# Performance work log

Measured on AMD Instinct MI355X. Metric: run time of the kernel, lower is better.

The kernel has to match this reference:

```python
import jax, jax.numpy as jnp
import numpy as np

N, T, NS, NO, HID, DENSE = 128, 1000, 10, 10, 64, 32


def setup_inputs() -> dict:
    key = jax.random.key(0)
    ks = jax.random.split(key, 16)
    s = 0.1  # init scale for RNN/dense weights
    inp = {
        "Yi_batch": jax.random.normal(ks[0], (N, T, NO), jnp.float32),
        "Xi_batch": jax.random.normal(ks[1], (N, T, NS), jnp.float32),
        # Kalman model parameters
        "H": 0.3 * jax.random.normal(ks[2], (NO, NS), jnp.float32),
        "mu_w": jnp.zeros((NO,), jnp.float32),
        "C_w": 0.1 * jnp.eye(NO, dtype=jnp.float32),
        # GRU parameters (torch layout: [3H, in])
        "W_ih": s * jax.random.normal(ks[3], (3 * HID, NO), jnp.float32),
        "W_hh": s * jax.random.normal(ks[4], (3 * HID, HID), jnp.float32),
        "b_ih": jnp.zeros((3 * HID,), jnp.float32),
        "b_hh": jnp.zeros((3 * HID,), jnp.float32),
        # dense head: fc -> relu -> {fc_mean, softplus(fc_vars)}
        "W_fc": s * jax.random.normal(ks[5], (DENSE, HID), jnp.float32),
        "b_fc": jnp.zeros((DENSE,), jnp.float32),
        "W_mean": s * jax.random.normal(ks[6], (NS, DENSE), jnp.float32),
        "b_mean": jnp.zeros((NS,), jnp.float32),
        "W_vars": s * jax.random.normal(ks[7], (NS, DENSE), jnp.float32),
        "b_vars": jnp.zeros((NS,), jnp.float32),
    }
    return inp


def _gru(x, W_ih, W_hh, b_ih, b_hh):
    # x: (N, T, in) -> (N, T, HID); torch GRU gate order: r, z, n
    xp = jnp.einsum('nti,gi->ntg', x, W_ih) + b_ih  # (N,T,3H)
    Hd = W_hh.shape[1]

    def step(h, xpt):
        gh = h @ W_hh.T + b_hh
        xr, xz, xn = jnp.split(xpt, 3, axis=-1)
        hr, hz, hn = jnp.split(gh, 3, axis=-1)
        r = jax.nn.sigmoid(xr + hr)
        z = jax.nn.sigmoid(xz + hz)
        n = jnp.tanh(xn + r * hn)
        h_new = (1.0 - z) * n + z * h
        return h_new, h_new

    h0 = jnp.zeros((x.shape[0], Hd), x.dtype)
    _, outs = jax.lax.scan(step, h0, jnp.swapaxes(xp, 0, 1))
    return jnp.swapaxes(outs, 0, 1)


def reference(Yi_batch, Xi_batch, H, mu_w, C_w,
              W_ih, W_hh, b_ih, b_hh,
              W_fc, b_fc, W_mean, b_mean, W_vars, b_vars):
    # --- RNN prior: mu_xt_yt_prev (N,T,NS), diagonal vars (N,T,NS) ---
    r_out = _gru(Yi_batch, W_ih, W_hh, b_ih, b_hh)
    y = jax.nn.relu(jnp.einsum('nth,dh->ntd', r_out, W_fc) + b_fc)
    mu_prev = jnp.einsum('ntd,sd->nts', y, W_mean) + b_mean          # (N,T,NS)
    vars_prev = jax.nn.softplus(jnp.einsum('ntd,sd->nts', y, W_vars) + b_vars)

    # --- posterior (Kalman update, L_prev diagonal) ---
    # S = H diag(v) H^T + C_w, per (n,t): (N,T,NO,NO)
    S = jnp.einsum('os,nts,ps->ntop', H, vars_prev, H) + C_w
    S_inv = jnp.linalg.inv(S)
    # K = diag(v) H^T S^{-1}: (N,T,NS,NO)
    K = jnp.einsum('nts,os,ntop->ntsp', vars_prev, H, S_inv)
    innov = Yi_batch - jnp.einsum('os,nts->nto', H, mu_prev)          # (N,T,NO)
    mu_post = mu_prev + jnp.einsum('ntso,nto->nts', K, innov)
    eye_s = jnp.eye(NS, dtype=vars_prev.dtype)
    L_post = vars_prev[..., :, None] * eye_s \
        - jnp.einsum('ntso,ntop,ntqp->ntsq', K, S, K)                 # (N,T,NS,NS)

    # --- Gaussian log-pdf of Xi_batch under N(mu_post, L_post) ---
    diff = Xi_batch - mu_post
    L_inv = jnp.linalg.inv(L_post)
    quad = jnp.einsum('nts,ntsq,ntq->nt', diff, L_inv, diff).sum(axis=1)
    logdet = jnp.linalg.slogdet(L_post)[1].sum(axis=1)
    # NOTE: faithful to source, including the + sign on the 2*pi term
    logprob = 0.5 * NS * T * jnp.log(jnp.asarray(2.0 * np.pi, diff.dtype)) \
        - 0.5 * logdet - 0.5 * quad                                   # (N,)
    return logprob.mean()
```

## Files before the change

kernel.cpp:

```cpp
#include <hip/hip_runtime.h>
#include <math.h>

#define N_    128
#define T_    1000
#define NS_   10
#define NO_   10
#define HID_  64
#define DENSE_ 32

typedef float v2f __attribute__((ext_vector_type(2)));
typedef float v4f __attribute__((ext_vector_type(4)));
typedef _Float16 h2v __attribute__((ext_vector_type(2)));

#define LDS_BARRIER() asm volatile("s_waitcnt lgkmcnt(0)\n\ts_barrier" ::: "memory")

#if __has_builtin(__builtin_amdgcn_fdot2)
#define FDOT2(acc, a, b) (acc) = __builtin_amdgcn_fdot2((a), (b), (acc), false)
#else
#define FDOT2(acc, a, b) asm("v_dot2_f32_f16 %0, %1, %2, %0" : "+v"(acc) : "v"(a), "v"(b))
#endif

__device__ __forceinline__ h2v pk_f16(float a, float b) {
    return __builtin_bit_cast(h2v, __builtin_amdgcn_cvt_pkrtz(a, b));
}

template <int CTRL>
__device__ __forceinline__ float dpp_mov(float x) {
    int r = __builtin_amdgcn_update_dpp(0, __builtin_bit_cast(int, x),
                                        CTRL, 0xF, 0xF, true);
    return __builtin_bit_cast(float, r);
}
__device__ __forceinline__ float quad_sum(float x) {
    x += dpp_mov<0xB1>(x);
    x += dpp_mov<0x4E>(x);
    return x;
}

__device__ __forceinline__ float fast_sigmoid(float x) {
    return __builtin_amdgcn_rcpf(1.f + __expf(-x));
}
__device__ __forceinline__ float fast_tanh(float x) {
    float e = __expf(2.f * x);
    return 1.f - 2.f * __builtin_amdgcn_rcpf(e + 1.f);
}

__global__ __launch_bounds__(256, 1) void gru_kernel(
    const float* __restrict__ Y,
    const float* __restrict__ W_ih,
    const float* __restrict__ W_hh,
    const float* __restrict__ b_ih,
    const float* __restrict__ b_hh,
    float* __restrict__ h_out,
    float* __restrict__ out)
{
    const int n    = blockIdx.x;
    const int tid  = threadIdx.x;
    const int w    = tid >> 6;
    const int l    = tid & 63;
    const int unit = w * 16 + (l >> 2);
    const int kh   = l & 3;

    if (n == 0 && tid == 0)
        out[0] = 0.5f * (float)NS_ * (float)T_ * logf(2.f * 3.14159265358979323846f);

    __shared__ __align__(16) h2v ylds[T_ * NO_ / 2];
    __shared__ __align__(16) _Float16 hbuf[HID_];

    const float* Yn = Y + (size_t)n * T_ * NO_;
    {
        const v2f* src = (const v2f*)Yn;
#pragma unroll 4
        for (int i = tid; i < T_ * NO_ / 2; i += 256) {
            v2f v = src[i];
            ylds[i] = pk_f16(v[0], v[1]);
        }
    }

    h2v whh[3][8];
#pragma unroll
    for (int g = 0; g < 3; ++g) {
        const v4f* wp = (const v4f*)(W_hh + (size_t)(g * HID_ + unit) * HID_ + kh * 16);
#pragma unroll
        for (int q = 0; q < 4; ++q) {
            v4f t = wp[q];
            whh[g][2 * q]     = pk_f16(t.x, t.y);
            whh[g][2 * q + 1] = pk_f16(t.z, t.w);
        }
    }
    h2v wihx[5];
    {
        const float s = (kh == 3) ? 0.f : 1.f;
        const int gx = (kh < 3) ? kh : 2;
        const v2f* ip = (const v2f*)(W_ih + (size_t)(gx * HID_ + unit) * NO_);
#pragma unroll
        for (int i = 0; i < 5; ++i) { v2f t = ip[i]; wihx[i] = pk_f16(t[0] * s, t[1] * s); }
    }
#pragma unroll
    for (int g = 0; g < 3; ++g)
#pragma unroll
        for (int k = 0; k < 8; ++k) asm volatile("" : "+v"(whh[g][k]));
#pragma unroll
    for (int i = 0; i < 5; ++i) asm volatile("" : "+v"(wihx[i]));

    const float mR = (kh == 0) ? 1.f : 0.f;
    const float mZ = (kh == 1) ? 1.f : 0.f;
    const float mN = (kh >= 2) ? 1.f : 0.f;
    const float cR = (kh == 0) ? (b_ih[unit] + b_hh[unit]) : 0.f;
    const float cZ = (kh == 0) ? (b_ih[HID_ + unit] + b_hh[HID_ + unit]) : 0.f;
    const float cN = (kh == 0) ? b_hh[2 * HID_ + unit] : 0.f;
    const float cX = (kh == 0) ? b_ih[2 * HID_ + unit] : 0.f;

    if (tid < HID_) hbuf[tid] = (_Float16)0.f;
    float h_own = 0.f;
    __syncthreads();

    float* hout = h_out + (size_t)n * T_ * HID_ + unit;

    h2v y0 = ylds[0], y1 = ylds[1], y2 = ylds[2], y3 = ylds[3], y4 = ylds[4];

    for (int t = 0; t < T_; ++t) {
        float xs = 0.f;
        FDOT2(xs, wihx[0], y0); FDOT2(xs, wihx[1], y1); FDOT2(xs, wihx[2], y2);
        FDOT2(xs, wihx[3], y3); FDOT2(xs, wihx[4], y4);

        float ar = cR, az = cZ, an = cN, xn = cX;
        const uint4* hp = (const uint4*)(hbuf + kh * 16);
        uint4 hq0 = hp[0], hq1 = hp[1];
        {
            h2v h0 = __builtin_bit_cast(h2v, hq0.x);
            h2v h1 = __builtin_bit_cast(h2v, hq0.y);
            h2v h2 = __builtin_bit_cast(h2v, hq0.z);
            h2v h3 = __builtin_bit_cast(h2v, hq0.w);
            FDOT2(ar, whh[0][0], h0); FDOT2(az, whh[1][0], h0); FDOT2(an, whh[2][0], h0);
            FDOT2(ar, whh[0][1], h1); FDOT2(az, whh[1][1], h1); FDOT2(an, whh[2][1], h1);
            FDOT2(ar, whh[0][2], h2); FDOT2(az, whh[1][2], h2); FDOT2(an, whh[2][2], h2);
            FDOT2(ar, whh[0][3], h3); FDOT2(az, whh[1][3], h3); FDOT2(an, whh[2][3], h3);
        }
        {
            h2v h0 = __builtin_bit_cast(h2v, hq1.x);
            h2v h1 = __builtin_bit_cast(h2v, hq1.y);
            h2v h2 = __builtin_bit_cast(h2v, hq1.z);
            h2v h3 = __builtin_bit_cast(h2v, hq1.w);
            FDOT2(ar, whh[0][4], h0); FDOT2(az, whh[1][4], h0); FDOT2(an, whh[2][4], h0);
            FDOT2(ar, whh[0][5], h1); FDOT2(az, whh[1][5], h1); FDOT2(an, whh[2][5], h1);
            FDOT2(ar, whh[0][6], h2); FDOT2(az, whh[1][6], h2); FDOT2(an, whh[2][6], h2);
            FDOT2(ar, whh[0][7], h3); FDOT2(az, whh[1][7], h3); FDOT2(an, whh[2][7], h3);
        }
        ar = fmaf(xs, mR, ar);
        az = fmaf(xs, mZ, az);
        xn = fmaf(xs, mN, xn);
        ar = quad_sum(ar);
        az = quad_sum(az);
        an = quad_sum(an);
        xn = quad_sum(xn);
        const float r  = fast_sigmoid(ar);
        const float z  = fast_sigmoid(az);
        const float nn = fast_tanh(xn + r * an);
        const float h_new = nn + z * (h_own - nn);
        h_own = h_new;
        if (kh == 0) {
            hbuf[unit] = (_Float16)h_new;
            hout[t * HID_] = h_new;
        }
        {
            const h2v* yrow = ylds + 5 * ((t + 1 < T_) ? t + 1 : t);
            y0 = yrow[0]; y1 = yrow[1]; y2 = yrow[2]; y3 = yrow[3]; y4 = yrow[4];
        }
        LDS_BARRIER();
    }
}

__global__ __launch_bounds__(256) void post_kernel(
    const float* __restrict__ h_out,
    const float* __restrict__ Y,
    const float* __restrict__ X,
    const float* __restrict__ Hm, const float* __restrict__ C_w,
    const float* __restrict__ W_fc, const float* __restrict__ b_fc,
    const float* __restrict__ W_mean, const float* __restrict__ b_mean,
    const float* __restrict__ W_vars, const float* __restrict__ b_vars,
    float* __restrict__ out)
{
    __shared__ float sWfc[DENSE_][HID_];
    __shared__ float sWm[NS_][DENSE_];
    __shared__ float sWv[NS_][DENSE_];
    __shared__ float sA[NS_][NO_];
    __shared__ float sM[NS_][NS_];
    __shared__ float sbfc[DENSE_], sbm[NS_], sbv[NS_];
    __shared__ float wsum[4];
    __shared__ float W[NO_][2 * NO_];
    __shared__ float fcol[NO_];

    const int tid = threadIdx.x;

    if (tid < NO_ * NO_) {
        const int i = tid / NO_, jj = tid % NO_;
        W[i][jj] = C_w[tid];
        W[i][NO_ + jj] = (i == jj) ? 1.f : 0.f;
    }
    __syncthreads();
    for (int p = 0; p < NO_; ++p) {
        const float ip = 1.f / W[p][p];
        __syncthreads();
        if (tid < 2 * NO_) W[p][tid] *= ip;
        __syncthreads();
        if (tid < NO_) fcol[tid] = (tid == p) ? 0.f : W[tid][p];
        __syncthreads();
        if (tid < NO_ * 2 * NO_) {
            const int i = tid / (2 * NO_), jj = tid % (2 * NO_);
            W[i][jj] -= fcol[i] * W[p][jj];
        }
        __syncthreads();
    }
    if (tid < NS_ * NO_) {
        const int s = tid / NO_, o = tid % NO_;
        float acc = 0.f;
        for (int p = 0; p < NO_; ++p) acc += Hm[p * NS_ + s] * W[p][NO_ + o];
        sA[s][o] = acc;
    }
    __syncthreads();
    if (tid < NS_ * NS_) {
        const int s = tid / NS_, q = tid % NS_;
        float acc = 0.f;
        for (int o = 0; o < NO_; ++o) acc += sA[s][o] * Hm[o * NS_ + q];
        sM[s][q] = acc;
    }

    for (int i = tid; i < DENSE_ * HID_; i += blockDim.x)
        sWfc[i / HID_][i % HID_] = W_fc[i];
    for (int i = tid; i < NS_ * DENSE_; i += blockDim.x) {
        sWm[i / DENSE_][i % DENSE_] = W_mean[i];
        sWv[i / DENSE_][i % DENSE_] = W_vars[i];
    }
    if (tid < DENSE_) sbfc[tid] = b_fc[tid];
    if (tid < NS_) { sbm[tid] = b_mean[tid]; sbv[tid] = b_vars[tid]; }
    __syncthreads();

    const int task = blockIdx.x * blockDim.x + tid;
    float contrib = 0.f;
    if (task < N_ * T_) {
        float y[DENSE_];
#pragma unroll
        for (int d = 0; d < DENSE_; ++d) y[d] = sbfc[d];
        const float* hp = h_out + (size_t)task * HID_;
#pragma unroll
        for (int k = 0; k < HID_; k += 4) {
            float4 h4 = *(const float4*)(hp + k);
#pragma unroll
            for (int d = 0; d < DENSE_; ++d) {
                y[d] += sWfc[d][k + 0] * h4.x + sWfc[d][k + 1] * h4.y +
                        sWfc[d][k + 2] * h4.z + sWfc[d][k + 3] * h4.w;
            }
        }
#pragma unroll
        for (int d = 0; d < DENSE_; ++d) y[d] = fmaxf(y[d], 0.f);

        float mu[NS_], vinv[NS_];
#pragma unroll
        for (int s = 0; s < NS_; ++s) {
            float am = sbm[s], av = sbv[s];
#pragma unroll
            for (int d = 0; d < DENSE_; ++d) { am += sWm[s][d] * y[d]; av += sWv[s][d] * y[d]; }
            mu[s] = am;
            float sp = (av > 20.f) ? av : log1pf(__expf(av));
            vinv[s] = 1.f / sp;
        }

        const float* yo = Y + (size_t)task * NO_;
        const float* xo = X + (size_t)task * NS_;
        float b[NS_];
#pragma unroll
        for (int s = 0; s < NS_; ++s) {
            float acc = vinv[s] * mu[s];
#pragma unroll
            for (int o = 0; o < NO_; ++o) acc += sA[s][o] * yo[o];
            b[s] = acc;
        }

        float L[NS_][NS_];
#pragma unroll
        for (int i = 0; i < NS_; ++i)
#pragma unroll
            for (int jj = 0; jj <= i; ++jj)
                L[i][jj] = sM[i][jj] + ((i == jj) ? vinv[i] : 0.f);
        float ld = 0.f;
        float dinv[NS_];
#pragma unroll
        for (int jj = 0; jj < NS_; ++jj) {
            float s = L[jj][jj];
#pragma unroll
            for (int k = 0; k < jj; ++k) s -= L[jj][k] * L[jj][k];
            float d = sqrtf(s);
            ld += __logf(d);
            float di = 1.f / d;
            dinv[jj] = di;
            L[jj][jj] = d;
#pragma unroll
            for (int i = jj + 1; i < NS_; ++i) {
                float t2 = L[i][jj];
#pragma unroll
                for (int k = 0; k < jj; ++k) t2 -= L[i][k] * L[jj][k];
                L[i][jj] = t2 * di;
            }
        }
        ld *= 2.f;

        float w[NS_];
#pragma unroll
        for (int i = 0; i < NS_; ++i) {
            float s = b[i];
#pragma unroll
            for (int k = 0; k < i; ++k) s -= L[i][k] * w[k];
            w[i] = s * dinv[i];
        }
        float mpost[NS_];
#pragma unroll
        for (int ii = NS_ - 1; ii >= 0; --ii) {
            float s = w[ii];
#pragma unroll
            for (int k = ii + 1; k < NS_; ++k) s -= L[k][ii] * mpost[k];
            mpost[ii] = s * dinv[ii];
        }

        float diff[NS_];
#pragma unroll
        for (int s = 0; s < NS_; ++s) diff[s] = xo[s] - mpost[s];
        float quad = 0.f;
#pragma unroll
        for (int jj = 0; jj < NS_; ++jj) {
            float u = 0.f;
#pragma unroll
            for (int i = jj; i < NS_; ++i) u += L[i][jj] * diff[i];
            quad += u * u;
        }

        contrib = 0.5f * (ld - quad) * (1.0f / (float)N_);
    }

#pragma unroll
    for (int off = 32; off; off >>= 1) contrib += __shfl_down(contrib, off);
    const int wid = tid >> 6;
    if ((tid & 63) == 0) wsum[wid] = contrib;
    __syncthreads();
    if (tid == 0) {
        float s = 0.f;
#pragma unroll
        for (int i = 0; i < 4; ++i) s += wsum[i];
        atomicAdd(out, s);
    }
}

extern "C" void kernel_launch(void* const* d_in, const int* in_sizes, int n_in,
                              void* d_out, int out_size, void* d_ws, size_t ws_size,
                              hipStream_t stream)
{
    const float* Y      = (const float*)d_in[0];
    const float* X      = (const float*)d_in[1];
    const float* H      = (const float*)d_in[2];
    const float* C_w    = (const float*)d_in[4];
    const float* W_ih   = (const float*)d_in[5];
    const float* W_hh   = (const float*)d_in[6];
    const float* b_ih   = (const float*)d_in[7];
    const float* b_hh   = (const float*)d_in[8];
    const float* W_fc   = (const float*)d_in[9];
    const float* b_fc   = (const float*)d_in[10];
    const float* W_mean = (const float*)d_in[11];
    const float* b_mean = (const float*)d_in[12];
    const float* W_vars = (const float*)d_in[13];
    const float* b_vars = (const float*)d_in[14];
    float* out = (float*)d_out;

    float* h_out = (float*)d_ws;

    hipLaunchKernelGGL(gru_kernel, dim3(N_), dim3(256), 0, stream,
                       Y, W_ih, W_hh, b_ih, b_hh, h_out, out);
    hipLaunchKernelGGL(post_kernel, dim3((N_ * T_ + 255) / 256), dim3(256), 0, stream,
                       h_out, Y, X, H, C_w, W_fc, b_fc, W_mean, b_mean,
                       W_vars, b_vars, out);
}
```

Measured before the change: 313.4 us.

## Pack two GRU sequences per 512-thread block sharing one barrier

Each GRU block now runs two batch sequences, one per 256-thread half, with separate LDS slices for Y and the hidden state. The grid drops from 128 to 64 blocks. The per-step workgroup barrier is now shared by 8 waves instead of 4, so each sequence can stall on the slower half. The intent is to put more waves per CU to hide the serial recurrence latency, or to pack sequences onto fewer CUs. On MI355X, which has more CUs than 128, this halves the number of active CUs and couples the two sequences through the barrier.

```diff
diff --git a/kernel.cpp b/kernel.cpp
--- a/kernel.cpp
+++ b/kernel.cpp
@@ -44,7 +44,7 @@
     return 1.f - 2.f * __builtin_amdgcn_rcpf(e + 1.f);
 }
 
-__global__ __launch_bounds__(256, 1) void gru_kernel(
+__global__ __launch_bounds__(512, 2) void gru_kernel(
     const float* __restrict__ Y,
     const float* __restrict__ W_ih,
     const float* __restrict__ W_hh,
@@ -53,26 +53,28 @@
     float* __restrict__ h_out,
     float* __restrict__ out)
 {
-    const int n    = blockIdx.x;
     const int tid  = threadIdx.x;
-    const int w    = tid >> 6;
-    const int l    = tid & 63;
+    const int sid  = tid >> 8;
+    const int t8   = tid & 255;
+    const int w    = t8 >> 6;
+    const int l    = t8 & 63;
     const int unit = w * 16 + (l >> 2);
     const int kh   = l & 3;
+    const int n    = 2 * blockIdx.x + sid;
 
     if (n == 0 && tid == 0)
         out[0] = 0.5f * (float)NS_ * (float)T_ * logf(2.f * 3.14159265358979323846f);
 
-    __shared__ __align__(16) h2v ylds[T_ * NO_ / 2];
-    __shared__ __align__(16) _Float16 hbuf[HID_];
+    __shared__ __align__(16) h2v ylds[2][T_ * NO_ / 2];
+    __shared__ __align__(16) _Float16 hbuf[2][HID_];
 
     const float* Yn = Y + (size_t)n * T_ * NO_;
     {
         const v2f* src = (const v2f*)Yn;
 #pragma unroll 4
-        for (int i = tid; i < T_ * NO_ / 2; i += 256) {
+        for (int i = t8; i < T_ * NO_ / 2; i += 256) {
             v2f v = src[i];
-            ylds[i] = pk_f16(v[0], v[1]);
+            ylds[sid][i] = pk_f16(v[0], v[1]);
         }
     }
 
@@ -110,13 +112,15 @@
     const float cN = (kh == 0) ? b_hh[2 * HID_ + unit] : 0.f;
     const float cX = (kh == 0) ? b_ih[2 * HID_ + unit] : 0.f;
 
-    if (tid < HID_) hbuf[tid] = (_Float16)0.f;
+    if (t8 < HID_) hbuf[sid][t8] = (_Float16)0.f;
     float h_own = 0.f;
     __syncthreads();
 
     float* hout = h_out + (size_t)n * T_ * HID_ + unit;
-
-    h2v y0 = ylds[0], y1 = ylds[1], y2 = ylds[2], y3 = ylds[3], y4 = ylds[4];
+    const h2v* yls = ylds[sid];
+    const _Float16* hb = hbuf[sid];
+
+    h2v y0 = yls[0], y1 = yls[1], y2 = yls[2], y3 = yls[3], y4 = yls[4];
 
     for (int t = 0; t < T_; ++t) {
         float xs = 0.f;
@@ -124,7 +128,7 @@
         FDOT2(xs, wihx[3], y3); FDOT2(xs, wihx[4], y4);
 
         float ar = cR, az = cZ, an = cN, xn = cX;
-        const uint4* hp = (const uint4*)(hbuf + kh * 16);
+        const uint4* hp = (const uint4*)(hb + kh * 16);
         uint4 hq0 = hp[0], hq1 = hp[1];
         {
             h2v h0 = __builtin_bit_cast(h2v, hq0.x);
@@ -159,11 +163,11 @@
         const float h_new = nn + z * (h_own - nn);
         h_own = h_new;
         if (kh == 0) {
-            hbuf[unit] = (_Float16)h_new;
+            hbuf[sid][unit] = (_Float16)h_new;
             hout[t * HID_] = h_new;
         }
         {
-            const h2v* yrow = ylds + 5 * ((t + 1 < T_) ? t + 1 : t);
+            const h2v* yrow = yls + 5 * ((t + 1 < T_) ? t + 1 : t);
             y0 = yrow[0]; y1 = yrow[1]; y2 = yrow[2]; y3 = yrow[3]; y4 = yrow[4];
         }
         LDS_BARRIER();
@@ -371,7 +375,7 @@
 
     float* h_out = (float*)d_ws;
 
-    hipLaunchKernelGGL(gru_kernel, dim3(N_), dim3(256), 0, stream,
+    hipLaunchKernelGGL(gru_kernel, dim3(N_ / 2), dim3(512), 0, stream,
                        Y, W_ih, W_hh, b_ih, b_hh, h_out, out);
     hipLaunchKernelGGL(post_kernel, dim3((N_ * T_ + 255) / 256), dim3(256), 0, stream,
                        h_out, Y, X, H, C_w, W_fc, b_fc, W_mean, b_mean,
```

Result: slower. 429.8 us (+37.1%).

## Store GRU hidden states as fp16 and hoist C_w inversion into setup kernel

Applied to the files above, without the earlier changes.

The GRU kernel now writes its hidden-state history in half precision, which halves the intermediate traffic written by the recurrence and read back by the post kernel. The small Gauss-Jordan inversion of C_w and the H-based constant products move out of every post_kernel block into a one-block setup kernel whose results the post kernel loads. This removes about 40 barrier-separated steps from each of the 500 post blocks, at the cost of an extra launch and fp16 rounding of the stored activations. The GRU already fed fp16 hidden state into its own recurrence, so the numerical change is limited to the dense head input.

```diff
diff --git a/kernel.cpp b/kernel.cpp
--- a/kernel.cpp
+++ b/kernel.cpp
@@ -44,14 +44,61 @@
     return 1.f - 2.f * __builtin_amdgcn_rcpf(e + 1.f);
 }
 
+__global__ void setup_consts(const float* __restrict__ H,
+                             const float* __restrict__ C_w,
+                             float* __restrict__ A,
+                             float* __restrict__ M,
+                             float* __restrict__ out)
+{
+    __shared__ float W[NO_][2 * NO_];
+    __shared__ float fcol[NO_];
+    __shared__ float As[NS_][NO_];
+    const int tid = threadIdx.x;
+    if (blockIdx.x != 0) return;
+    if (tid == 0)
+        out[0] = 0.5f * (float)NS_ * (float)T_ * logf(2.f * 3.14159265358979323846f);
+    if (tid < NO_ * NO_) {
+        const int i = tid / NO_, j = tid % NO_;
+        W[i][j] = C_w[tid];
+        W[i][NO_ + j] = (i == j) ? 1.f : 0.f;
+    }
+    __syncthreads();
+    for (int p = 0; p < NO_; ++p) {
+        const float ip = 1.f / W[p][p];
+        __syncthreads();
+        if (tid < 2 * NO_) W[p][tid] *= ip;
+        __syncthreads();
+        if (tid < NO_) fcol[tid] = (tid == p) ? 0.f : W[tid][p];
+        __syncthreads();
+        if (tid < NO_ * 2 * NO_) {
+            const int i = tid / (2 * NO_), j = tid % (2 * NO_);
+            W[i][j] -= fcol[i] * W[p][j];
+        }
+        __syncthreads();
+    }
+    if (tid < NS_ * NO_) {
+        const int s = tid / NO_, o = tid % NO_;
+        float acc = 0.f;
+        for (int p = 0; p < NO_; ++p) acc += H[p * NS_ + s] * W[p][NO_ + o];
+        As[s][o] = acc;
+        A[tid] = acc;
+    }
+    __syncthreads();
+    if (tid < NS_ * NS_) {
+        const int s = tid / NS_, q = tid % NS_;
+        float acc = 0.f;
+        for (int o = 0; o < NO_; ++o) acc += As[s][o] * H[o * NS_ + q];
+        M[tid] = acc;
+    }
+}
+
 __global__ __launch_bounds__(256, 1) void gru_kernel(
     const float* __restrict__ Y,
     const float* __restrict__ W_ih,
     const float* __restrict__ W_hh,
     const float* __restrict__ b_ih,
     const float* __restrict__ b_hh,
-    float* __restrict__ h_out,
-    float* __restrict__ out)
+    _Float16* __restrict__ h_out)
 {
     const int n    = blockIdx.x;
     const int tid  = threadIdx.x;
@@ -60,9 +107,6 @@
     const int unit = w * 16 + (l >> 2);
     const int kh   = l & 3;
 
-    if (n == 0 && tid == 0)
-        out[0] = 0.5f * (float)NS_ * (float)T_ * logf(2.f * 3.14159265358979323846f);
-
     __shared__ __align__(16) h2v ylds[T_ * NO_ / 2];
     __shared__ __align__(16) _Float16 hbuf[HID_];
 
@@ -114,7 +158,7 @@
     float h_own = 0.f;
     __syncthreads();
 
-    float* hout = h_out + (size_t)n * T_ * HID_ + unit;
+    _Float16* hout = h_out + (size_t)n * T_ * HID_ + unit;
 
     h2v y0 = ylds[0], y1 = ylds[1], y2 = ylds[2], y3 = ylds[3], y4 = ylds[4];
 
@@ -159,8 +203,9 @@
         const float h_new = nn + z * (h_own - nn);
         h_own = h_new;
         if (kh == 0) {
-            hbuf[unit] = (_Float16)h_new;
-            hout[t * HID_] = h_new;
+            const _Float16 hf = (_Float16)h_new;
+            hbuf[unit] = hf;
+            hout[t * HID_] = hf;
         }
         {
             const h2v* yrow = ylds + 5 * ((t + 1 < T_) ? t + 1 : t);
@@ -171,13 +216,14 @@
 }
 
 __global__ __launch_bounds__(256) void post_kernel(
-    const float* __restrict__ h_out,
+    const _Float16* __restrict__ h_out,
     const float* __restrict__ Y,
     const float* __restrict__ X,
-    const float* __restrict__ Hm, const float* __restrict__ C_w,
     const float* __restrict__ W_fc, const float* __restrict__ b_fc,
     const float* __restrict__ W_mean, const float* __restrict__ b_mean,
     const float* __restrict__ W_vars, const float* __restrict__ b_vars,
+    const float* __restrict__ Ac,
+    const float* __restrict__ Mc,
     float* __restrict__ out)
 {
     __shared__ float sWfc[DENSE_][HID_];
@@ -187,43 +233,8 @@
     __shared__ float sM[NS_][NS_];
     __shared__ float sbfc[DENSE_], sbm[NS_], sbv[NS_];
     __shared__ float wsum[4];
-    __shared__ float W[NO_][2 * NO_];
-    __shared__ float fcol[NO_];
 
     const int tid = threadIdx.x;
-
-    if (tid < NO_ * NO_) {
-        const int i = tid / NO_, jj = tid % NO_;
-        W[i][jj] = C_w[tid];
-        W[i][NO_ + jj] = (i == jj) ? 1.f : 0.f;
-    }
-    __syncthreads();
-    for (int p = 0; p < NO_; ++p) {
-        const float ip = 1.f / W[p][p];
-        __syncthreads();
-        if (tid < 2 * NO_) W[p][tid] *= ip;
-        __syncthreads();
-        if (tid < NO_) fcol[tid] = (tid == p) ? 0.f : W[tid][p];
-        __syncthreads();
-        if (tid < NO_ * 2 * NO_) {
-            const int i = tid / (2 * NO_), jj = tid % (2 * NO_);
-            W[i][jj] -= fcol[i] * W[p][jj];
-        }
-        __syncthreads();
-    }
-    if (tid < NS_ * NO_) {
-        const int s = tid / NO_, o = tid % NO_;
-        float acc = 0.f;
-        for (int p = 0; p < NO_; ++p) acc += Hm[p * NS_ + s] * W[p][NO_ + o];
-        sA[s][o] = acc;
-    }
-    __syncthreads();
-    if (tid < NS_ * NS_) {
-        const int s = tid / NS_, q = tid % NS_;
-        float acc = 0.f;
-        for (int o = 0; o < NO_; ++o) acc += sA[s][o] * Hm[o * NS_ + q];
-        sM[s][q] = acc;
-    }
 
     for (int i = tid; i < DENSE_ * HID_; i += blockDim.x)
         sWfc[i / HID_][i % HID_] = W_fc[i];
@@ -231,6 +242,8 @@
         sWm[i / DENSE_][i % DENSE_] = W_mean[i];
         sWv[i / DENSE_][i % DENSE_] = W_vars[i];
     }
+    for (int i = tid; i < NS_ * NO_; i += blockDim.x) sA[i / NO_][i % NO_] = Ac[i];
+    for (int i = tid; i < NS_ * NS_; i += blockDim.x) sM[i / NS_][i % NS_] = Mc[i];
     if (tid < DENSE_) sbfc[tid] = b_fc[tid];
     if (tid < NS_) { sbm[tid] = b_mean[tid]; sbv[tid] = b_vars[tid]; }
     __syncthreads();
@@ -241,14 +254,25 @@
         float y[DENSE_];
 #pragma unroll
         for (int d = 0; d < DENSE_; ++d) y[d] = sbfc[d];
-        const float* hp = h_out + (size_t)task * HID_;
-#pragma unroll
-        for (int k = 0; k < HID_; k += 4) {
-            float4 h4 = *(const float4*)(hp + k);
+        const uint4* hp4 = (const uint4*)(h_out + (size_t)task * HID_);
+#pragma unroll
+        for (int q = 0; q < 8; ++q) {
+            uint4 hq = hp4[q];
+            h2v p0 = __builtin_bit_cast(h2v, hq.x);
+            h2v p1 = __builtin_bit_cast(h2v, hq.y);
+            h2v p2 = __builtin_bit_cast(h2v, hq.z);
+            h2v p3 = __builtin_bit_cast(h2v, hq.w);
+            const float h0 = (float)p0[0], h1 = (float)p0[1];
+            const float h2 = (float)p1[0], h3 = (float)p1[1];
+            const float h4 = (float)p2[0], h5 = (float)p2[1];
+            const float h6 = (float)p3[0], h7 = (float)p3[1];
+            const int k = 8 * q;
 #pragma unroll
             for (int d = 0; d < DENSE_; ++d) {
-                y[d] += sWfc[d][k + 0] * h4.x + sWfc[d][k + 1] * h4.y +
-                        sWfc[d][k + 2] * h4.z + sWfc[d][k + 3] * h4.w;
+                y[d] += sWfc[d][k + 0] * h0 + sWfc[d][k + 1] * h1 +
+                        sWfc[d][k + 2] * h2 + sWfc[d][k + 3] * h3 +
+                        sWfc[d][k + 4] * h4 + sWfc[d][k + 5] * h5 +
+                        sWfc[d][k + 6] * h6 + sWfc[d][k + 7] * h7;
             }
         }
 #pragma unroll
@@ -369,11 +393,14 @@
     const float* b_vars = (const float*)d_in[14];
     float* out = (float*)d_out;
 
-    float* h_out = (float*)d_ws;
-
+    _Float16* h_out = (_Float16*)d_ws;
+    float* Ac = (float*)((char*)d_ws + (size_t)N_ * T_ * HID_ * sizeof(_Float16));
+    float* Mc = Ac + NS_ * NO_;
+
+    hipLaunchKernelGGL(setup_consts, dim3(1), dim3(256), 0, stream, H, C_w, Ac, Mc, out);
     hipLaunchKernelGGL(gru_kernel, dim3(N_), dim3(256), 0, stream,
-                       Y, W_ih, W_hh, b_ih, b_hh, h_out, out);
+                       Y, W_ih, W_hh, b_ih, b_hh, h_out);
     hipLaunchKernelGGL(post_kernel, dim3((N_ * T_ + 255) / 256), dim3(256), 0, stream,
-                       h_out, Y, X, H, C_w, W_fc, b_fc, W_mean, b_mean,
-                       W_vars, b_vars, out);
-}
+                       h_out, Y, X, W_fc, b_fc, W_mean, b_mean, W_vars, b_vars,
+                       Ac, Mc, out);
+}
```

New measurement: 320.8 us. 2.4% more time.
